# Optimization experiments

Hardware: AMD Instinct MI355X
Metric: run time of the kernel (lower is better)

The kernel has to match this reference:

```python
import jax, jax.numpy as jnp
import numpy as np

B = 262144
STEPS = 15            # Program.steps = var(15)
SPEED = 5.0           # Program.straight_speed
TRAJ_IDX = np.array([10, 1, 2, 3, 4, 5, 6, 7, 8, 17])
FEAT_IDX = np.array([1, 2, 3, 4, 9, 17])


def setup_inputs() -> dict:
    key = jax.random.key(0)
    ks = jax.random.split(key, 9)
    x = jax.random.normal(ks[0], (B, 18), dtype=jnp.float32)
    x = x.at[:, 0].set(0.0)  # loop counter i starts at 0 -> exactly 15 iterations
    return {
        "x": x,
        "c1w": jax.random.normal(ks[1], (2,), jnp.float32) * 0.5,
        "c1b": jax.random.normal(ks[2], (1,), jnp.float32) * 0.1,
        "c2w": jax.random.normal(ks[3], (2,), jnp.float32) * 0.5,
        "c2b": jax.random.normal(ks[4], (1,), jnp.float32) * 0.1,
        "l1w": jax.random.normal(ks[5], (4, 32), jnp.float32) * 0.3,
        "l1b": jax.random.normal(ks[6], (32,), jnp.float32) * 0.1,
        "l2w": jax.random.normal(ks[7], (32, 5), jnp.float32) * 0.3,
        "l2b": jax.random.normal(ks[8], (5,), jnp.float32) * 0.1,
    }


def _classifier(feat, c1w, c1b, c2w, c2b, l1w, l1b, l2w, l2b):
    # feat: [B,6] -> conv1d(k=2): [B,5] -> conv1d(k=2): [B,4] -> 32 -> 5, sigmoid
    h = jax.nn.relu(c1w[0] * feat[:, :-1] + c1w[1] * feat[:, 1:] + c1b)
    h = jax.nn.relu(c2w[0] * h[:, :-1] + c2w[1] * h[:, 1:] + c2b)
    h = jax.nn.relu(h @ l1w + l1b)
    return jax.nn.sigmoid(h @ l2w + l2b)  # [B,5]


def _distance(s):
    return (s[:, 1] - s[:, 3]) ** 2 + (s[:, 2] - s[:, 4]) ** 2


def _program(x, c1w, c1b, c2w, c2b, l1w, l1b, l2w, l2b):
    s = x.at[:, 10].set(_distance(x))          # initial assign_distance
    traj0 = s[:, TRAJ_IDX]                      # initial trajectory_update

    def step(s, _):
        # assign_branch_probability
        p = _classifier(s[:, FEAT_IDX], c1w, c1b, c2w, c2b, l1w, l1b, l2w, l2b)
        s = (s.at[:, 5].set(p[:, 0]).at[:, 6].set(p[:, 1]).at[:, 7].set(p[:, 2])
              .at[:, 8].set(p[:, 3]).at[:, 17].set(p[:, 4]))
        p5, p6, p7, p8 = p[:, 0], p[:, 1], p[:, 2], p[:, 3]
        # assign_comparison_block: pairwise diffs a..f at indices 11..16
        a, b, c = p6 - p5, p7 - p5, p8 - p5
        d, e, f = p7 - p6, p8 - p6, p8 - p7
        s = (s.at[:, 11].set(a).at[:, 12].set(b).at[:, 13].set(c)
              .at[:, 14].set(d).at[:, 15].set(e).at[:, 16].set(f))
        # ifelse_argmax_ITE: nested compare against comparison_bar=0.0
        dx_c = jnp.where(c <= 0.0, 0.0, SPEED);  st_c = jnp.where(c <= 0.0, 0.0, 3.0)   # cruise vs right
        dx_f = jnp.where(f <= 0.0, 0.0, SPEED);  st_f = jnp.where(f <= 0.0, 2.0, 3.0)   # straight vs right
        dx_e = jnp.where(e <= 0.0, -SPEED, SPEED); st_e = jnp.where(e <= 0.0, 1.0, 3.0)  # left vs right
        dx_b = jnp.where(b <= 0.0, dx_c, dx_f);  st_b = jnp.where(b <= 0.0, st_c, st_f)
        dx_d = jnp.where(d <= 0.0, dx_e, dx_f);  st_d = jnp.where(d <= 0.0, st_e, st_f)
        dx   = jnp.where(a <= 0.0, dx_b, dx_d);  st   = jnp.where(a <= 0.0, st_b, st_d)
        s = s.at[:, 1].add(dx).at[:, 9].set(st)
        # assign_y1, assign_x2, assign_update_i, assign_distance
        s = s.at[:, 2].add(SPEED).at[:, 3].add(SPEED).at[:, 0].add(1.0)
        s = s.at[:, 10].set(_distance(s))
        return s, s[:, TRAJ_IDX]

    s, recs = jax.lax.scan(step, s, None, length=STEPS)
    traj = jnp.concatenate([traj0[:, None, :], jnp.moveaxis(recs, 0, 1)], axis=1)  # [B,16,10]
    return jnp.concatenate([s, traj.reshape(s.shape[0], -1)], axis=1)  # [B, 18+160]


def reference(x, c1w, c1b, c2w, c2b, l1w, l1b, l2w, l2b):
    return _program(x, c1w, c1b, c2w, c2b, l1w, l1b, l2w, l2b)
```

## Files before the change

### kernel.cpp

```cpp
#include <hip/hip_runtime.h>


constexpr int kB     = 262144;
constexpr int kSteps = 15;
constexpr int PAD    = 33;
constexpr int WOFF   = 256 * PAD;

__device__ __forceinline__ float relu_(float v) { return fmaxf(v, 0.0f); }
__device__ __forceinline__ float sigmoid_(float v) {
    return __builtin_amdgcn_rcpf(1.0f + __expf(-v));
}

__global__ __launch_bounds__(256, 1) void Program_4578435138231_kernel(
    const float* __restrict__ x,
    const float* __restrict__ c1w, const float* __restrict__ c1b,
    const float* __restrict__ c2w, const float* __restrict__ c2b,
    const float* __restrict__ l1w, const float* __restrict__ l1b,
    const float* __restrict__ l2w, const float* __restrict__ l2b,
    float* __restrict__ out)
{
    __shared__ __align__(16) float lds[256 * PAD + 32 * 12];
    const int tid = threadIdx.x;
    const int R0  = blockIdx.x * 256;

    if (tid < 32) {
        const int k = tid;
        float* w = lds + WOFF + k * 12;
        w[0] = l1w[k];          w[1] = l1w[32 + k];
        w[2] = l1w[64 + k];     w[3] = l1w[96 + k];
        w[4] = l1b[k];
        w[5] = l2w[5 * k + 0];  w[6] = l2w[5 * k + 1];
        w[7] = l2w[5 * k + 2];  w[8] = l2w[5 * k + 3];
        w[9] = l2w[5 * k + 4];
    }

    {
        const float* xblk = x + (size_t)R0 * 18;
        #pragma unroll
        for (int j = 0; j < 18; ++j) {
            int flat = tid + 256 * j;
            float v  = xblk[flat];
            int r = (int)(((unsigned)flat * 58255u) >> 20);
            int c = flat - r * 18;
            lds[r * PAD + c] = v;
        }
    }
    __syncthreads();
    float s[18];
    #pragma unroll
    for (int j = 0; j < 18; ++j) s[j] = lds[tid * PAD + j];

    const float* wl = lds + WOFF;
    float wA[32], wB[32], wC[32], wD[32], wE[32];
    float wF[32], wG[32], wH[32], wI[32], wJ[32];
    #pragma unroll
    for (int k = 0; k < 32; ++k) {
        float4 a = *reinterpret_cast<const float4*>(wl + k * 12);
        float4 b = *reinterpret_cast<const float4*>(wl + k * 12 + 4);
        float2 c = *reinterpret_cast<const float2*>(wl + k * 12 + 8);
        wA[k] = a.x; wB[k] = a.y; wC[k] = a.z; wD[k] = a.w; wE[k] = b.x;
        wF[k] = b.y; wG[k] = b.z; wH[k] = b.w; wI[k] = c.x; wJ[k] = c.y;
    }
    #pragma unroll
    for (int k = 0; k < 32; ++k) {
        asm volatile("" : "+v"(wA[k]), "+v"(wB[k]), "+v"(wC[k]), "+v"(wD[k]),
                          "+v"(wE[k]), "+v"(wF[k]), "+v"(wG[k]), "+v"(wH[k]),
                          "+v"(wI[k]), "+v"(wJ[k]));
    }
    __syncthreads();

    const float cw10 = c1w[0], cw11 = c1w[1], cb1 = c1b[0];
    const float cw20 = c2w[0], cw21 = c2w[1], cb2 = c2b[0];
    const float b20 = l2b[0], b21 = l2b[1], b22 = l2b[2], b23 = l2b[3], b24 = l2b[4];

    {
        float dA = s[1] - s[3], dB = s[2] - s[4];
        s[10] = dA * dA + dB * dB;
    }

    float* lr = lds + tid * PAD;

    auto flush32 = [&](int wcol) {
        __syncthreads();
        const int rr = tid >> 5, cc = tid & 31;
        const float* lp = lds + rr * PAD + cc;
        float*       op = out + (size_t)(R0 + rr) * 178 + wcol + cc;
        #pragma unroll
        for (int j = 0; j < 32; ++j) {
            op[(size_t)(8 * j) * 178] = lp[8 * j * PAD];
        }
        __syncthreads();
    };

    int wstart = 18;
    int nextb  = 50;

    lr[0] = s[10]; lr[1] = s[1];  lr[2] = s[2]; lr[3] = s[3]; lr[4] = s[4];
    lr[5] = s[5];  lr[6] = s[6];  lr[7] = s[7]; lr[8] = s[8]; lr[9] = s[17];

    #pragma unroll 1
    for (int t = 0; t < kSteps; ++t) {
        float f0 = s[1], f1 = s[2], f2 = s[3], f3 = s[4], f4 = s[9], f5 = s[17];
        float h10 = relu_(cw10 * f0 + cw11 * f1 + cb1);
        float h11 = relu_(cw10 * f1 + cw11 * f2 + cb1);
        float h12 = relu_(cw10 * f2 + cw11 * f3 + cb1);
        float h13 = relu_(cw10 * f3 + cw11 * f4 + cb1);
        float h14 = relu_(cw10 * f4 + cw11 * f5 + cb1);
        float g0 = relu_(cw20 * h10 + cw21 * h11 + cb2);
        float g1 = relu_(cw20 * h11 + cw21 * h12 + cb2);
        float g2 = relu_(cw20 * h12 + cw21 * h13 + cb2);
        float g3 = relu_(cw20 * h13 + cw21 * h14 + cb2);

        float p0 = b20, p1 = b21, p2 = b22, p3 = b23, p4 = b24;
        #pragma unroll
        for (int k = 0; k < 32; ++k) {
            float h = g0 * wA[k] + g1 * wB[k] + g2 * wC[k]
                    + g3 * wD[k] + wE[k];
            h = relu_(h);
            p0 += h * wF[k];
            p1 += h * wG[k];
            p2 += h * wH[k];
            p3 += h * wI[k];
            p4 += h * wJ[k];
        }
        p0 = sigmoid_(p0); p1 = sigmoid_(p1); p2 = sigmoid_(p2);
        p3 = sigmoid_(p3); p4 = sigmoid_(p4);

        s[5] = p0; s[6] = p1; s[7] = p2; s[8] = p3; s[17] = p4;
        float a = p1 - p0, b = p2 - p0, c = p3 - p0;
        float d = p2 - p1, e = p3 - p1, f = p3 - p2;
        s[11] = a; s[12] = b; s[13] = c; s[14] = d; s[15] = e; s[16] = f;

        float dx_c = (c <= 0.f) ? 0.f  : 5.f,  st_c = (c <= 0.f) ? 0.f : 3.f;
        float dx_f = (f <= 0.f) ? 0.f  : 5.f,  st_f = (f <= 0.f) ? 2.f : 3.f;
        float dx_e = (e <= 0.f) ? -5.f : 5.f,  st_e = (e <= 0.f) ? 1.f : 3.f;
        float dx_b = (b <= 0.f) ? dx_c : dx_f, st_b = (b <= 0.f) ? st_c : st_f;
        float dx_d = (d <= 0.f) ? dx_e : dx_f, st_d = (d <= 0.f) ? st_e : st_f;
        float dx   = (a <= 0.f) ? dx_b : dx_d, st   = (a <= 0.f) ? st_b : st_d;

        s[1] += dx; s[9] = st;
        s[2] += 5.f; s[3] += 5.f; s[0] += 1.f;
        float dA = s[1] - s[3], dB = s[2] - s[4];
        s[10] = dA * dA + dB * dB;

        float v0 = s[10], v1 = s[1], v2 = s[2], v3 = s[3], v4 = s[4];
        float v5 = s[5],  v6 = s[6], v7 = s[7], v8 = s[8], v9 = s[17];
        const int c0 = 28 + 10 * t;
        const int kk = nextb - c0;
        int off = c0 - wstart;
        if (kk >= 10) {
            lr[off + 0] = v0; lr[off + 1] = v1; lr[off + 2] = v2;
            lr[off + 3] = v3; lr[off + 4] = v4; lr[off + 5] = v5;
            lr[off + 6] = v6; lr[off + 7] = v7; lr[off + 8] = v8;
            lr[off + 9] = v9;
            if (kk == 10) {
                flush32(wstart);
                wstart = nextb; nextb += 32;
            }
        } else {
            if (kk > 0) lr[off + 0] = v0;
            if (kk > 1) lr[off + 1] = v1;
            if (kk > 2) lr[off + 2] = v2;
            if (kk > 3) lr[off + 3] = v3;
            if (kk > 4) lr[off + 4] = v4;
            if (kk > 5) lr[off + 5] = v5;
            if (kk > 6) lr[off + 6] = v6;
            if (kk > 7) lr[off + 7] = v7;
            if (kk > 8) lr[off + 8] = v8;
            if (kk > 9) lr[off + 9] = v9;
            flush32(wstart);
            wstart = nextb; nextb += 32;
            off = c0 - wstart;
            if (kk <= 0) lr[off + 0] = v0;
            if (kk <= 1) lr[off + 1] = v1;
            if (kk <= 2) lr[off + 2] = v2;
            if (kk <= 3) lr[off + 3] = v3;
            if (kk <= 4) lr[off + 4] = v4;
            if (kk <= 5) lr[off + 5] = v5;
            if (kk <= 6) lr[off + 6] = v6;
            if (kk <= 7) lr[off + 7] = v7;
            if (kk <= 8) lr[off + 8] = v8;
            if (kk <= 9) lr[off + 9] = v9;
        }
    }

    __syncthreads();
    #pragma unroll
    for (int j = 0; j < 18; ++j) lr[j] = s[j];
    __syncthreads();
    #pragma unroll
    for (int j = 0; j < 18; ++j) {
        int flat = tid + 256 * j;
        int r = (int)(((unsigned)flat * 58255u) >> 20);
        int c = flat - r * 18;
        out[(size_t)(R0 + r) * 178 + c] = lds[r * PAD + c];
    }
}

extern "C" void kernel_launch(void* const* d_in, const int* in_sizes, int n_in,
                              void* d_out, int out_size, void* d_ws, size_t ws_size,
                              hipStream_t stream) {
    const float* x   = (const float*)d_in[0];
    const float* c1w = (const float*)d_in[1];
    const float* c1b = (const float*)d_in[2];
    const float* c2w = (const float*)d_in[3];
    const float* c2b = (const float*)d_in[4];
    const float* l1w = (const float*)d_in[5];
    const float* l1b = (const float*)d_in[6];
    const float* l2w = (const float*)d_in[7];
    const float* l2b = (const float*)d_in[8];
    float* out = (float*)d_out;

    Program_4578435138231_kernel<<<kB / 256, 256, 0, stream>>>(
        x, c1w, c1b, c2w, c2b, l1w, l1b, l2w, l2b, out);
}
```

Before: 287.6 us.

## Split each row's hidden layer across two threads with shuffle reduction

Each row is now processed by a pair of lanes, each holding half of the 32 hidden units' weights in registers. The partial output sums are combined with a lane-xor shuffle. This halves per-thread register use and doubles the thread count per row, which should raise occupancy (launch bounds now ask for 2 blocks per CU) and latency hiding. The cost is duplicated conv/branch arithmetic in both lanes, shuffle overhead, and twice as many blocks, each running the LDS staging and flush barriers.

Result: faster. 267.8 us, median of 2 (-6.9%).

```diff
diff --git a/kernel.cpp b/kernel.cpp
--- a/kernel.cpp
+++ b/kernel.cpp
@@ -4,14 +4,15 @@
 constexpr int kB     = 262144;
 constexpr int kSteps = 15;
 constexpr int PAD    = 33;
-constexpr int WOFF   = 256 * PAD;
+constexpr int RPB    = 128;
+constexpr int WOFF   = RPB * PAD;
 
 __device__ __forceinline__ float relu_(float v) { return fmaxf(v, 0.0f); }
 __device__ __forceinline__ float sigmoid_(float v) {
     return __builtin_amdgcn_rcpf(1.0f + __expf(-v));
 }
 
-__global__ __launch_bounds__(256, 1) void Program_4578435138231_kernel(
+__global__ __launch_bounds__(256, 2) void Program_4578435138231_kernel(
     const float* __restrict__ x,
     const float* __restrict__ c1w, const float* __restrict__ c1b,
     const float* __restrict__ c2w, const float* __restrict__ c2b,
@@ -19,9 +20,11 @@
     const float* __restrict__ l2w, const float* __restrict__ l2b,
     float* __restrict__ out)
 {
-    __shared__ __align__(16) float lds[256 * PAD + 32 * 12];
-    const int tid = threadIdx.x;
-    const int R0  = blockIdx.x * 256;
+    __shared__ __align__(16) float lds[RPB * PAD + 32 * 12];
+    const int tid  = threadIdx.x;
+    const int rid  = tid >> 1;
+    const int half = tid & 1;
+    const int R0   = blockIdx.x * RPB;
 
     if (tid < 32) {
         const int k = tid;
@@ -37,7 +40,7 @@
     {
         const float* xblk = x + (size_t)R0 * 18;
         #pragma unroll
-        for (int j = 0; j < 18; ++j) {
+        for (int j = 0; j < 9; ++j) {
             int flat = tid + 256 * j;
             float v  = xblk[flat];
             int r = (int)(((unsigned)flat * 58255u) >> 20);
@@ -48,13 +51,13 @@
     __syncthreads();
     float s[18];
     #pragma unroll
-    for (int j = 0; j < 18; ++j) s[j] = lds[tid * PAD + j];
-
-    const float* wl = lds + WOFF;
-    float wA[32], wB[32], wC[32], wD[32], wE[32];
-    float wF[32], wG[32], wH[32], wI[32], wJ[32];
-    #pragma unroll
-    for (int k = 0; k < 32; ++k) {
+    for (int j = 0; j < 18; ++j) s[j] = lds[rid * PAD + j];
+
+    const float* wl = lds + WOFF + half * (16 * 12);
+    float wA[16], wB[16], wC[16], wD[16], wE[16];
+    float wF[16], wG[16], wH[16], wI[16], wJ[16];
+    #pragma unroll
+    for (int k = 0; k < 16; ++k) {
         float4 a = *reinterpret_cast<const float4*>(wl + k * 12);
         float4 b = *reinterpret_cast<const float4*>(wl + k * 12 + 4);
         float2 c = *reinterpret_cast<const float2*>(wl + k * 12 + 8);
@@ -62,7 +65,7 @@
         wF[k] = b.y; wG[k] = b.z; wH[k] = b.w; wI[k] = c.x; wJ[k] = c.y;
     }
     #pragma unroll
-    for (int k = 0; k < 32; ++k) {
+    for (int k = 0; k < 16; ++k) {
         asm volatile("" : "+v"(wA[k]), "+v"(wB[k]), "+v"(wC[k]), "+v"(wD[k]),
                           "+v"(wE[k]), "+v"(wF[k]), "+v"(wG[k]), "+v"(wH[k]),
                           "+v"(wI[k]), "+v"(wJ[k]));
@@ -71,14 +74,17 @@
 
     const float cw10 = c1w[0], cw11 = c1w[1], cb1 = c1b[0];
     const float cw20 = c2w[0], cw21 = c2w[1], cb2 = c2b[0];
-    const float b20 = l2b[0], b21 = l2b[1], b22 = l2b[2], b23 = l2b[3], b24 = l2b[4];
+    const float b20 = half ? 0.f : l2b[0], b21 = half ? 0.f : l2b[1];
+    const float b22 = half ? 0.f : l2b[2], b23 = half ? 0.f : l2b[3];
+    const float b24 = half ? 0.f : l2b[4];
 
     {
         float dA = s[1] - s[3], dB = s[2] - s[4];
         s[10] = dA * dA + dB * dB;
     }
 
-    float* lr = lds + tid * PAD;
+    float* lr = lds + rid * PAD;
+    auto rec = [&](int idx, float v) { if (!half) lr[idx] = v; };
 
     auto flush32 = [&](int wcol) {
         __syncthreads();
@@ -86,7 +92,7 @@
         const float* lp = lds + rr * PAD + cc;
         float*       op = out + (size_t)(R0 + rr) * 178 + wcol + cc;
         #pragma unroll
-        for (int j = 0; j < 32; ++j) {
+        for (int j = 0; j < 16; ++j) {
             op[(size_t)(8 * j) * 178] = lp[8 * j * PAD];
         }
         __syncthreads();
@@ -95,8 +101,8 @@
     int wstart = 18;
     int nextb  = 50;
 
-    lr[0] = s[10]; lr[1] = s[1];  lr[2] = s[2]; lr[3] = s[3]; lr[4] = s[4];
-    lr[5] = s[5];  lr[6] = s[6];  lr[7] = s[7]; lr[8] = s[8]; lr[9] = s[17];
+    rec(0, s[10]); rec(1, s[1]);  rec(2, s[2]); rec(3, s[3]); rec(4, s[4]);
+    rec(5, s[5]);  rec(6, s[6]);  rec(7, s[7]); rec(8, s[8]); rec(9, s[17]);
 
     #pragma unroll 1
     for (int t = 0; t < kSteps; ++t) {
@@ -113,7 +119,7 @@
 
         float p0 = b20, p1 = b21, p2 = b22, p3 = b23, p4 = b24;
         #pragma unroll
-        for (int k = 0; k < 32; ++k) {
+        for (int k = 0; k < 16; ++k) {
             float h = g0 * wA[k] + g1 * wB[k] + g2 * wC[k]
                     + g3 * wD[k] + wE[k];
             h = relu_(h);
@@ -123,6 +129,12 @@
             p3 += h * wI[k];
             p4 += h * wJ[k];
         }
+        p0 += __shfl_xor(p0, 1, 64);
+        p1 += __shfl_xor(p1, 1, 64);
+        p2 += __shfl_xor(p2, 1, 64);
+        p3 += __shfl_xor(p3, 1, 64);
+        p4 += __shfl_xor(p4, 1, 64);
+
         p0 = sigmoid_(p0); p1 = sigmoid_(p1); p2 = sigmoid_(p2);
         p3 = sigmoid_(p3); p4 = sigmoid_(p4);
 
@@ -149,47 +161,49 @@
         const int kk = nextb - c0;
         int off = c0 - wstart;
         if (kk >= 10) {
-            lr[off + 0] = v0; lr[off + 1] = v1; lr[off + 2] = v2;
-            lr[off + 3] = v3; lr[off + 4] = v4; lr[off + 5] = v5;
-            lr[off + 6] = v6; lr[off + 7] = v7; lr[off + 8] = v8;
-            lr[off + 9] = v9;
+            rec(off + 0, v0); rec(off + 1, v1); rec(off + 2, v2);
+            rec(off + 3, v3); rec(off + 4, v4); rec(off + 5, v5);
+            rec(off + 6, v6); rec(off + 7, v7); rec(off + 8, v8);
+            rec(off + 9, v9);
             if (kk == 10) {
                 flush32(wstart);
                 wstart = nextb; nextb += 32;
             }
         } else {
-            if (kk > 0) lr[off + 0] = v0;
-            if (kk > 1) lr[off + 1] = v1;
-            if (kk > 2) lr[off + 2] = v2;
-            if (kk > 3) lr[off + 3] = v3;
-            if (kk > 4) lr[off + 4] = v4;
-            if (kk > 5) lr[off + 5] = v5;
-            if (kk > 6) lr[off + 6] = v6;
-            if (kk > 7) lr[off + 7] = v7;
-            if (kk > 8) lr[off + 8] = v8;
-            if (kk > 9) lr[off + 9] = v9;
+            if (kk > 0) rec(off + 0, v0);
+            if (kk > 1) rec(off + 1, v1);
+            if (kk > 2) rec(off + 2, v2);
+            if (kk > 3) rec(off + 3, v3);
+            if (kk > 4) rec(off + 4, v4);
+            if (kk > 5) rec(off + 5, v5);
+            if (kk > 6) rec(off + 6, v6);
+            if (kk > 7) rec(off + 7, v7);
+            if (kk > 8) rec(off + 8, v8);
+            if (kk > 9) rec(off + 9, v9);
             flush32(wstart);
             wstart = nextb; nextb += 32;
             off = c0 - wstart;
-            if (kk <= 0) lr[off + 0] = v0;
-            if (kk <= 1) lr[off + 1] = v1;
-            if (kk <= 2) lr[off + 2] = v2;
-            if (kk <= 3) lr[off + 3] = v3;
-            if (kk <= 4) lr[off + 4] = v4;
-            if (kk <= 5) lr[off + 5] = v5;
-            if (kk <= 6) lr[off + 6] = v6;
-            if (kk <= 7) lr[off + 7] = v7;
-            if (kk <= 8) lr[off + 8] = v8;
-            if (kk <= 9) lr[off + 9] = v9;
-        }
-    }
-
-    __syncthreads();
-    #pragma unroll
-    for (int j = 0; j < 18; ++j) lr[j] = s[j];
-    __syncthreads();
-    #pragma unroll
-    for (int j = 0; j < 18; ++j) {
+            if (kk <= 0) rec(off + 0, v0);
+            if (kk <= 1) rec(off + 1, v1);
+            if (kk <= 2) rec(off + 2, v2);
+            if (kk <= 3) rec(off + 3, v3);
+            if (kk <= 4) rec(off + 4, v4);
+            if (kk <= 5) rec(off + 5, v5);
+            if (kk <= 6) rec(off + 6, v6);
+            if (kk <= 7) rec(off + 7, v7);
+            if (kk <= 8) rec(off + 8, v8);
+            if (kk <= 9) rec(off + 9, v9);
+        }
+    }
+
+    __syncthreads();
+    if (!half) {
+        #pragma unroll
+        for (int j = 0; j < 18; ++j) lr[j] = s[j];
+    }
+    __syncthreads();
+    #pragma unroll
+    for (int j = 0; j < 9; ++j) {
         int flat = tid + 256 * j;
         int r = (int)(((unsigned)flat * 58255u) >> 20);
         int c = flat - r * 18;
@@ -211,6 +225,6 @@
     const float* l2b = (const float*)d_in[8];
     float* out = (float*)d_out;
 
-    Program_4578435138231_kernel<<<kB / 256, 256, 0, stream>>>(
+    Program_4578435138231_kernel<<<kB / RPB, 256, 0, stream>>>(
         x, c1w, c1b, c2w, c2b, l1w, l1b, l2w, l2b, out);
 }
```
